# Kernel optimization log

Measured on AMD Instinct MI355X. Metric: run time of the kernel, lower is better.

Reference implementation:

```python
import jax, jax.numpy as jnp
import numpy as np

MG = (5, 5)          # mesh_grid_size
UP = (17, 17)        # upsample_size
IMG = (512.0, 512.0) # image_size
B = 8192
FC_OUT = MG[0] * MG[1] * 2  # 50
KH = (UP[0] - 1) // (MG[0] - 1) + 1  # 5
KW = (UP[1] - 1) // (MG[1] - 1) + 1  # 5
SH = (UP[0] - 1) // (MG[0] - 1)      # 4
SW = (UP[1] - 1) // (MG[1] - 1)      # 4
L0 = MG[0] - 1
L1 = MG[1] - 1


def _grid(h, w):
    # channel 0: x coords vary along rows (image_size[0]); channel 1: y along cols
    x_t = jnp.broadcast_to(jnp.linspace(0.0, IMG[0], h)[:, None], (h, w))
    y_t = jnp.broadcast_to(jnp.linspace(0.0, IMG[1], w)[None, :], (h, w))
    return jnp.stack([x_t, y_t], 0)  # [2, h, w]


def _unfold22(a):
    # a: [B, 2, H, W] -> [B, (H-1)*(W-1), 4, 2]; 4 = kernel positions row-major, 2 = channel
    p = jnp.stack([a[:, :, :-1, :-1], a[:, :, :-1, 1:],
                   a[:, :, 1:, :-1], a[:, :, 1:, 1:]], axis=2)  # [B,2,4,H-1,W-1]
    return p.reshape(a.shape[0], 2, 4, -1).transpose(0, 3, 2, 1)


def _persp(src, dst):
    # exact 4-point homography solve (torchgeometry.get_perspective_transform)
    x0, y0 = src[..., 0], src[..., 1]
    u, v = dst[..., 0], dst[..., 1]
    z = jnp.zeros_like(x0)
    o = jnp.ones_like(x0)
    ax = jnp.stack([x0, y0, o, z, z, z, -u * x0, -u * y0], -1)  # [N,4,8]
    ay = jnp.stack([z, z, z, x0, y0, o, -v * x0, -v * y0], -1)
    A = jnp.concatenate([ax, ay], 1)                 # [N,8,8]
    bb = jnp.concatenate([u, v], 1)[..., None]       # [N,8,1]
    h = jnp.linalg.solve(A, bb)[..., 0]              # [N,8]
    return jnp.concatenate([h, o[:, :1]], 1).reshape(-1, 3, 3)


def setup_inputs() -> dict:
    key = jax.random.key(0)
    ks = jax.random.split(key, 4)
    def lin(k, i, o):
        return jax.random.normal(k, (i, o), jnp.float32) / jnp.sqrt(i)
    return {
        "x": jax.random.normal(ks[0], (B, 1024), jnp.float32),
        "W1": lin(ks[1], 1024, 1024), "b1": jnp.zeros((1024,), jnp.float32),
        "W2": lin(ks[2], 1024, 2048), "b2": jnp.zeros((2048,), jnp.float32),
        "W3": lin(ks[3], 2048, FC_OUT), "b3": jnp.zeros((FC_OUT,), jnp.float32),
    }


def reference(x, W1, b1, W2, b2, W3, b3):
    Bn = x.shape[0]
    h = jax.nn.relu(x @ W1 + b1)
    h = jax.nn.relu(h @ W2 + b2)
    out = (h @ W3 + b3).reshape(Bn, 2, MG[0], MG[1])  # [B,2,5,5] mesh flow

    # sparse control grid and 2x2 patch corner points
    gs = _grid(MG[0], MG[1])
    src = _unfold22(jnp.broadcast_to(gs[None], (Bn, 2, MG[0], MG[1]))).reshape(-1, 4, 2)
    flow = _unfold22(out).reshape(-1, 4, 2)
    M = _persp(src, src + flow)  # [B*16, 3, 3]

    # dense grid and its unfold2 (kernel KHxKW, stride SHxSW) patch points
    gd = _grid(UP[0], UP[1])  # [2, 17, 17]
    gi = (np.arange(L0) * SH)[:, None, None, None] + np.arange(KH)[None, None, :, None]
    gj = (np.arange(L1) * SW)[None, :, None, None] + np.arange(KW)[None, None, None, :]
    I, J = np.broadcast_arrays(gi, gj)  # [L0,L1,KH,KW]
    pts = gd[:, I, J].transpose(1, 2, 3, 4, 0).reshape(1, L0 * L1, KH * KW, 2)
    pts = jnp.broadcast_to(pts, (Bn, L0 * L1, KH * KW, 2)).reshape(Bn * L0 * L1, KH * KW, 2)

    # transform_points: homogeneous warp + perspective divide
    ph = jnp.concatenate([pts, jnp.ones(pts.shape[:-1] + (1,), pts.dtype)], -1)
    oh = jnp.einsum('nij,npj->npi', M, ph)
    warped = oh[..., :2] / oh[..., 2:3]
    warped = warped.reshape(Bn, L0, L1, KH, KW, 2)

    # Fold: scatter-accumulate overlapping patches
    fold = jnp.zeros((Bn, 2, UP[0], UP[1]), x.dtype)
    for i in range(L0):
        for j in range(L1):
            blk = warped[:, i, j].transpose(0, 3, 1, 2)  # [B,2,KH,KW]
            fold = fold.at[:, :, i * SH:i * SH + KH, j * SW:j * SW + KW].add(blk)

    # boundary rescaling exactly as the torch code: only the 5x5 crossing points
    idx = np.arange(0, UP[0], MG[0] - 1)
    X, Y = np.meshgrid(idx, idx, indexing='xy')
    fold = fold.at[:, :, X, Y].multiply(0.5)
    for (a, b) in ((0, 0), (0, UP[1] - 1), (UP[0] - 1, UP[1] - 1), (UP[0] - 1, 0)):
        fold = fold.at[:, :, a, b].multiply(2.0)

    return fold - gd[None]  # upsampled mesh flow [B,2,17,17]
```

## Files before the change

### kernel.cpp

```cpp
#include <hip/hip_runtime.h>

typedef __bf16 bf16x8 __attribute__((ext_vector_type(8)));
typedef float f32x4 __attribute__((ext_vector_type(4)));

__device__ __forceinline__ unsigned short f2bf(float f) {
  unsigned int u = __builtin_bit_cast(unsigned int, f);
  unsigned int r = (u + 0x7fffu + ((u >> 16) & 1u)) >> 16;
  return (unsigned short)r;
}

__device__ __forceinline__ void load16_lds(const unsigned short* g, unsigned short* l) {
  __builtin_amdgcn_global_load_lds(
      (const __attribute__((address_space(1))) void*)g,
      (__attribute__((address_space(3))) void*)l, 16, 0, 0);
}


__global__ __launch_bounds__(256) void prepass(
    const float* __restrict__ x, const float* __restrict__ W1,
    const float* __restrict__ W2, const float* __restrict__ W3,
    unsigned short* __restrict__ xbf, unsigned short* __restrict__ w1t,
    unsigned short* __restrict__ w2t, unsigned short* __restrict__ w3t) {
  __shared__ float tile[32][33];
  const int bid = blockIdx.x;
  const int t = threadIdx.x;
  if (bid < 2048) {
    for (int i = bid * 256 + t; i < 2097152; i += 2048 * 256) {
      float4 f = ((const float4*)x)[i];
      uint2 o;
      o.x = (unsigned)f2bf(f.x) | ((unsigned)f2bf(f.y) << 16);
      o.y = (unsigned)f2bf(f.z) | ((unsigned)f2bf(f.w) << 16);
      ((uint2*)xbf)[i] = o;
    }
  } else if (bid < 3072) {
    int ti = bid - 2048;
    int n0 = (ti & 31) * 32, k0 = (ti >> 5) * 32;
    int tx = t & 31, ty = t >> 5;
    #pragma unroll
    for (int r = 0; r < 32; r += 8)
      tile[ty + r][tx] = W1[(size_t)(k0 + ty + r) * 1024 + n0 + tx];
    __syncthreads();
    #pragma unroll
    for (int r = 0; r < 32; r += 8)
      w1t[(size_t)(n0 + ty + r) * 1024 + k0 + tx] = f2bf(tile[tx][ty + r]);
  } else if (bid < 5120) {
    int ti = bid - 3072;
    int n0 = (ti & 63) * 32, k0 = (ti >> 6) * 32;
    int tx = t & 31, ty = t >> 5;
    #pragma unroll
    for (int r = 0; r < 32; r += 8)
      tile[ty + r][tx] = W2[(size_t)(k0 + ty + r) * 2048 + n0 + tx];
    __syncthreads();
    #pragma unroll
    for (int r = 0; r < 32; r += 8)
      w2t[(size_t)(n0 + ty + r) * 1024 + k0 + tx] = f2bf(tile[tx][ty + r]);
  } else {
    int idx = (bid - 5120) * 256 + t;
    int n = idx >> 11, k = idx & 2047;
    w3t[idx] = f2bf((n < 50) ? W3[(size_t)k * 50 + n] : 0.f);
  }
}


__global__ __launch_bounds__(256) void gemm_bt_relu(
    const unsigned short* __restrict__ A,
    const unsigned short* __restrict__ Bt,
    const float* __restrict__ bias,
    unsigned short* __restrict__ C,
    int N, int K) {
  __shared__ __align__(16) unsigned short As[128 * 64];
  __shared__ __align__(16) unsigned short Bs[128 * 64];
  const int t = threadIdx.x;
  const int m0 = blockIdx.x * 128;
  const int n0 = blockIdx.y * 128;
  const int lane = t & 63, wv = t >> 6;
  const int l16 = lane & 15, quad = lane >> 4;
  const int wm = (wv >> 1) * 64, wn = (wv & 1) * 64;

  const int srow = t >> 3;
  const int scol = ((t & 7) ^ (srow & 7)) * 8;
  const unsigned short* Ag0 = A + (size_t)(m0 + srow) * K + scol;
  const unsigned short* Bg0 = Bt + (size_t)(n0 + srow) * K + scol;
  unsigned short* AsW = As + wv * 8 * 64;
  unsigned short* BsW = Bs + wv * 8 * 64;

  f32x4 acc[4][4] = {};

  for (int k0 = 0; k0 < K; k0 += 64) {
    #pragma unroll
    for (int r = 0; r < 4; ++r) {
      load16_lds(Ag0 + (size_t)(r * 32) * K + k0, AsW + r * 32 * 64);
      load16_lds(Bg0 + (size_t)(r * 32) * K + k0, BsW + r * 32 * 64);
    }
    __syncthreads();
    #pragma unroll
    for (int half = 0; half < 2; ++half) {
      bf16x8 af[4], bfr[4];
      #pragma unroll
      for (int mi = 0; mi < 4; ++mi) {
        int row = wm + mi * 16 + l16;
        int pb = (half * 4 + quad) ^ (row & 7);
        af[mi] = *(const bf16x8*)&As[row * 64 + pb * 8];
      }
      #pragma unroll
      for (int ni = 0; ni < 4; ++ni) {
        int row = wn + ni * 16 + l16;
        int pb = (half * 4 + quad) ^ (row & 7);
        bfr[ni] = *(const bf16x8*)&Bs[row * 64 + pb * 8];
      }
      #pragma unroll
      for (int mi = 0; mi < 4; ++mi)
        #pragma unroll
        for (int ni = 0; ni < 4; ++ni)
          acc[mi][ni] = __builtin_amdgcn_mfma_f32_16x16x32_bf16(
              af[mi], bfr[ni], acc[mi][ni], 0, 0, 0);
    }
    __syncthreads();
  }

  #pragma unroll
  for (int mi = 0; mi < 4; ++mi) {
    #pragma unroll
    for (int ni = 0; ni < 4; ++ni) {
      int col = n0 + wn + ni * 16 + l16;
      float bv = bias[col];
      #pragma unroll
      for (int r = 0; r < 4; ++r) {
        int row = m0 + wm + mi * 16 + quad * 4 + r;
        float v = acc[mi][ni][r] + bv;
        v = fmaxf(v, 0.f);
        C[(size_t)row * N + col] = f2bf(v);
      }
    }
  }
}


__global__ __launch_bounds__(256) void gemm_bt_relu_n64(
    const unsigned short* __restrict__ A,
    const unsigned short* __restrict__ Bt,
    const float* __restrict__ bias,
    unsigned short* __restrict__ C,
    int N, int K) {
  __shared__ __align__(16) unsigned short As[128 * 64];
  __shared__ __align__(16) unsigned short Bs[64 * 64];
  const int t = threadIdx.x;
  const int m0 = blockIdx.x * 128;
  const int n0 = blockIdx.y * 64;
  const int lane = t & 63, wv = t >> 6;
  const int l16 = lane & 15, quad = lane >> 4;
  const int wm = (wv >> 1) * 64, wn = (wv & 1) * 32;

  const int srow = t >> 3;
  const int scol = ((t & 7) ^ (srow & 7)) * 8;
  const unsigned short* Ag0 = A + (size_t)(m0 + srow) * K + scol;
  const unsigned short* Bg0 = Bt + (size_t)(n0 + srow) * K + scol;
  unsigned short* AsW = As + wv * 8 * 64;
  unsigned short* BsW = Bs + wv * 8 * 64;

  f32x4 acc[4][2] = {};

  for (int k0 = 0; k0 < K; k0 += 64) {
    #pragma unroll
    for (int r = 0; r < 4; ++r)
      load16_lds(Ag0 + (size_t)(r * 32) * K + k0, AsW + r * 32 * 64);
    #pragma unroll
    for (int r = 0; r < 2; ++r)
      load16_lds(Bg0 + (size_t)(r * 32) * K + k0, BsW + r * 32 * 64);
    __syncthreads();
    #pragma unroll
    for (int half = 0; half < 2; ++half) {
      bf16x8 af[4], bfr[2];
      #pragma unroll
      for (int mi = 0; mi < 4; ++mi) {
        int row = wm + mi * 16 + l16;
        int pb = (half * 4 + quad) ^ (row & 7);
        af[mi] = *(const bf16x8*)&As[row * 64 + pb * 8];
      }
      #pragma unroll
      for (int ni = 0; ni < 2; ++ni) {
        int row = wn + ni * 16 + l16;
        int pb = (half * 4 + quad) ^ (row & 7);
        bfr[ni] = *(const bf16x8*)&Bs[row * 64 + pb * 8];
      }
      #pragma unroll
      for (int mi = 0; mi < 4; ++mi)
        #pragma unroll
        for (int ni = 0; ni < 2; ++ni)
          acc[mi][ni] = __builtin_amdgcn_mfma_f32_16x16x32_bf16(
              af[mi], bfr[ni], acc[mi][ni], 0, 0, 0);
    }
    __syncthreads();
  }

  #pragma unroll
  for (int mi = 0; mi < 4; ++mi) {
    #pragma unroll
    for (int ni = 0; ni < 2; ++ni) {
      int col = n0 + wn + ni * 16 + l16;
      float bv = bias[col];
      #pragma unroll
      for (int r = 0; r < 4; ++r) {
        int row = m0 + wm + mi * 16 + quad * 4 + r;
        float v = acc[mi][ni][r] + bv;
        v = fmaxf(v, 0.f);
        C[(size_t)row * N + col] = f2bf(v);
      }
    }
  }
}


__global__ __launch_bounds__(256) void gemm3_geom(
    const unsigned short* __restrict__ A,
    const unsigned short* __restrict__ Bt,
    const float* __restrict__ b3,
    float* __restrict__ outp) {
  __shared__ __align__(16) unsigned short As[16 * 64];
  __shared__ __align__(16) unsigned short Bs[64 * 64];
  __shared__ float s_out3[16 * 64];
  __shared__ float s_bias[64];
  __shared__ float fold[16 * 578];
  const int t = threadIdx.x;
  const int lane = t & 63, wv = t >> 6;
  const int l16 = lane & 15, quad = lane >> 4;
  const int m0 = blockIdx.x * 16;

  if (t < 64) s_bias[t] = (t < 50) ? b3[t] : 0.f;
  for (int i = t; i < 16 * 578; i += 256) fold[i] = 0.f;

  const int srow = lane >> 3;
  const int sg = lane & 7;

  f32x4 acc = {};

  for (int k0 = 0; k0 < 2048; k0 += 64) {
    if (wv < 2) {
      int row = wv * 8 + srow;
      int col = (sg ^ (row & 7)) * 8;
      load16_lds(A + (size_t)(m0 + row) * 2048 + k0 + col, As + wv * 8 * 64);
    }
    #pragma unroll
    for (int r = 0; r < 2; ++r) {
      int row = wv * 16 + r * 8 + srow;
      int col = (sg ^ (row & 7)) * 8;
      load16_lds(Bt + (size_t)row * 2048 + k0 + col, Bs + (wv * 16 + r * 8) * 64);
    }
    __syncthreads();
    #pragma unroll
    for (int half = 0; half < 2; ++half) {
      int apb = (half * 4 + quad) ^ (l16 & 7);
      bf16x8 af = *(const bf16x8*)&As[l16 * 64 + apb * 8];
      int brow = wv * 16 + l16;
      int bpb = (half * 4 + quad) ^ (brow & 7);
      bf16x8 bf = *(const bf16x8*)&Bs[brow * 64 + bpb * 8];
      acc = __builtin_amdgcn_mfma_f32_16x16x32_bf16(af, bf, acc, 0, 0, 0);
    }
    __syncthreads();
  }

  {
    int n = wv * 16 + l16;
    float bv = s_bias[n];
    #pragma unroll
    for (int r = 0; r < 4; ++r)
      s_out3[(quad * 4 + r) * 64 + n] = acc[r] + bv;
  }
  __syncthreads();

  {
    const int bl = t >> 4;
    const int p = t & 15;
    const int pi = p >> 2, pj = p & 3;
    const float* o = &s_out3[bl * 64];

    float u00 = 128.f * pi       + o[pi * 5 + pj];
    float v00 = 128.f * pj       + o[25 + pi * 5 + pj];
    float u01 = 128.f * pi       + o[pi * 5 + pj + 1];
    float v01 = 128.f * (pj + 1) + o[25 + pi * 5 + pj + 1];
    float u10 = 128.f * (pi + 1) + o[(pi + 1) * 5 + pj];
    float v10 = 128.f * pj       + o[25 + (pi + 1) * 5 + pj];
    float u11 = 128.f * (pi + 1) + o[(pi + 1) * 5 + pj + 1];
    float v11 = 128.f * (pj + 1) + o[25 + (pi + 1) * 5 + pj + 1];

    float sx = u00 - u10 + u11 - u01;
    float sy = v00 - v10 + v11 - v01;
    float dx1 = u10 - u11, dx2 = u01 - u11;
    float dy1 = v10 - v11, dy2 = v01 - v11;
    float rden = 1.f / (dx1 * dy2 - dx2 * dy1);
    float g = (sx * dy2 - dx2 * sy) * rden;
    float h = (dx1 * sy - sx * dy1) * rden;
    float a = u10 - u00 + g * u10;
    float b = u01 - u00 + h * u01;
    float c = u00;
    float d = v10 - v00 + g * v10;
    float e = v01 - v00 + h * v01;
    float f = v00;

    #pragma unroll
    for (int ai = 0; ai < 5; ++ai) {
      #pragma unroll
      for (int bi = 0; bi < 5; ++bi) {
        float s = 0.25f * ai, tt = 0.25f * bi;
        float rw = 1.f / (g * s + h * tt + 1.f);
        float xx = (a * s + b * tt + c) * rw;
        float yy = (d * s + e * tt + f) * rw;
        int gi = pi * 4 + ai, gj = pj * 4 + bi;
        atomicAdd(&fold[(bl * 2 + 0) * 289 + gi * 17 + gj], xx);
        atomicAdd(&fold[(bl * 2 + 1) * 289 + gi * 17 + gj], yy);
      }
    }
  }
  __syncthreads();

  for (int i = t; i < 16 * 578; i += 256) {
    int blb = i / 578;
    int rem = i - blb * 578;
    int ch = rem / 289;
    int ij = rem - ch * 289;
    int gi = ij / 17, gj = ij - gi * 17;
    float val = fold[i];
    if ((gi % 4 == 0) && (gj % 4 == 0)) val *= 0.5f;
    if ((gi == 0 || gi == 16) && (gj == 0 || gj == 16)) val *= 2.f;
    val -= (ch == 0) ? 32.f * gi : 32.f * gj;
    outp[(size_t)(m0 + blb) * 578 + rem] = val;
  }
}


extern "C" void kernel_launch(void* const* d_in, const int* in_sizes, int n_in,
                              void* d_out, int out_size, void* d_ws, size_t ws_size,
                              hipStream_t stream) {
  const float* x  = (const float*)d_in[0];
  const float* W1 = (const float*)d_in[1];
  const float* b1 = (const float*)d_in[2];
  const float* W2 = (const float*)d_in[3];
  const float* b2 = (const float*)d_in[4];
  const float* W3 = (const float*)d_in[5];
  const float* b3 = (const float*)d_in[6];
  float* outp = (float*)d_out;

  char* ws = (char*)d_ws;
  size_t off = 0;
  auto alloc = [&](size_t bytes) {
    void* pp = ws + off;
    off += (bytes + 255) & ~(size_t)255;
    return pp;
  };
  unsigned short* xbf = (unsigned short*)alloc((size_t)8192 * 1024 * 2);
  unsigned short* w1t = (unsigned short*)alloc((size_t)1024 * 1024 * 2);
  unsigned short* w2t = (unsigned short*)alloc((size_t)2048 * 1024 * 2);
  unsigned short* w3t = (unsigned short*)alloc((size_t)64 * 2048 * 2);
  unsigned short* h1  = (unsigned short*)alloc((size_t)8192 * 1024 * 2);
  unsigned short* h2  = (unsigned short*)alloc((size_t)8192 * 2048 * 2);

  prepass<<<5632, 256, 0, stream>>>(x, W1, W2, W3, xbf, w1t, w2t, w3t);

  gemm_bt_relu_n64<<<dim3(64, 16), 256, 0, stream>>>(xbf, w1t, b1, h1, 1024, 1024);
  gemm_bt_relu<<<dim3(64, 16), 256, 0, stream>>>(h1, w2t, b2, h2, 2048, 1024);
  gemm3_geom<<<512, 256, 0, stream>>>(h2, w3t, b3, outp);
}
```

Before: 219.3 us.

## Split third GEMM into split-K tiled kernel plus separate geometry reduce kernel

```diff
diff --git a/kernel.cpp b/kernel.cpp
--- a/kernel.cpp
+++ b/kernel.cpp
@@ -211,60 +211,92 @@
 }
 
 
-__global__ __launch_bounds__(256) void gemm3_geom(
+__global__ __launch_bounds__(256) void gemm3_part(
     const unsigned short* __restrict__ A,
     const unsigned short* __restrict__ Bt,
-    const float* __restrict__ b3,
-    float* __restrict__ outp) {
-  __shared__ __align__(16) unsigned short As[16 * 64];
+    float* __restrict__ part) {
+  __shared__ __align__(16) unsigned short As[128 * 64];
   __shared__ __align__(16) unsigned short Bs[64 * 64];
-  __shared__ float s_out3[16 * 64];
-  __shared__ float s_bias[64];
-  __shared__ float fold[16 * 578];
-  const int t = threadIdx.x;
+  const int t = threadIdx.x;
+  const int m0 = blockIdx.x * 128;
+  const int kz = blockIdx.y;
   const int lane = t & 63, wv = t >> 6;
   const int l16 = lane & 15, quad = lane >> 4;
-  const int m0 = blockIdx.x * 16;
-
-  if (t < 64) s_bias[t] = (t < 50) ? b3[t] : 0.f;
+  const int wm = (wv >> 1) * 64, wn = (wv & 1) * 32;
+
+  const int srow = t >> 3;
+  const int scol = ((t & 7) ^ (srow & 7)) * 8;
+  const unsigned short* Ag0 = A + (size_t)(m0 + srow) * 2048 + kz * 512 + scol;
+  const unsigned short* Bg0 = Bt + (size_t)srow * 2048 + kz * 512 + scol;
+  unsigned short* AsW = As + wv * 8 * 64;
+  unsigned short* BsW = Bs + wv * 8 * 64;
+
+  f32x4 acc[4][2] = {};
+
+  for (int k0 = 0; k0 < 512; k0 += 64) {
+    #pragma unroll
+    for (int r = 0; r < 4; ++r)
+      load16_lds(Ag0 + (size_t)(r * 32) * 2048 + k0, AsW + r * 32 * 64);
+    #pragma unroll
+    for (int r = 0; r < 2; ++r)
+      load16_lds(Bg0 + (size_t)(r * 32) * 2048 + k0, BsW + r * 32 * 64);
+    __syncthreads();
+    #pragma unroll
+    for (int half = 0; half < 2; ++half) {
+      bf16x8 af[4], bfr[2];
+      #pragma unroll
+      for (int mi = 0; mi < 4; ++mi) {
+        int row = wm + mi * 16 + l16;
+        int pb = (half * 4 + quad) ^ (row & 7);
+        af[mi] = *(const bf16x8*)&As[row * 64 + pb * 8];
+      }
+      #pragma unroll
+      for (int ni = 0; ni < 2; ++ni) {
+        int row = wn + ni * 16 + l16;
+        int pb = (half * 4 + quad) ^ (row & 7);
+        bfr[ni] = *(const bf16x8*)&Bs[row * 64 + pb * 8];
+      }
+      #pragma unroll
+      for (int mi = 0; mi < 4; ++mi)
+        #pragma unroll
+        for (int ni = 0; ni < 2; ++ni)
+          acc[mi][ni] = __builtin_amdgcn_mfma_f32_16x16x32_bf16(
+              af[mi], bfr[ni], acc[mi][ni], 0, 0, 0);
+    }
+    __syncthreads();
+  }
+
+  float* pbase = part + (size_t)kz * 8192 * 64;
+  #pragma unroll
+  for (int mi = 0; mi < 4; ++mi) {
+    #pragma unroll
+    for (int ni = 0; ni < 2; ++ni) {
+      int col = wn + ni * 16 + l16;
+      #pragma unroll
+      for (int r = 0; r < 4; ++r) {
+        int row = m0 + wm + mi * 16 + quad * 4 + r;
+        pbase[(size_t)row * 64 + col] = acc[mi][ni][r];
+      }
+    }
+  }
+}
+
+
+__global__ __launch_bounds__(256) void geom_reduce(
+    const float* __restrict__ part, const float* __restrict__ b3,
+    float* __restrict__ outp) {
+  __shared__ float s_out3[16 * 64];
+  __shared__ float fold[16 * 578];
+  const int t = threadIdx.x;
+  const int bbase = blockIdx.x * 16;
+
   for (int i = t; i < 16 * 578; i += 256) fold[i] = 0.f;
-
-  const int srow = lane >> 3;
-  const int sg = lane & 7;
-
-  f32x4 acc = {};
-
-  for (int k0 = 0; k0 < 2048; k0 += 64) {
-    if (wv < 2) {
-      int row = wv * 8 + srow;
-      int col = (sg ^ (row & 7)) * 8;
-      load16_lds(A + (size_t)(m0 + row) * 2048 + k0 + col, As + wv * 8 * 64);
-    }
-    #pragma unroll
-    for (int r = 0; r < 2; ++r) {
-      int row = wv * 16 + r * 8 + srow;
-      int col = (sg ^ (row & 7)) * 8;
-      load16_lds(Bt + (size_t)row * 2048 + k0 + col, Bs + (wv * 16 + r * 8) * 64);
-    }
-    __syncthreads();
-    #pragma unroll
-    for (int half = 0; half < 2; ++half) {
-      int apb = (half * 4 + quad) ^ (l16 & 7);
-      bf16x8 af = *(const bf16x8*)&As[l16 * 64 + apb * 8];
-      int brow = wv * 16 + l16;
-      int bpb = (half * 4 + quad) ^ (brow & 7);
-      bf16x8 bf = *(const bf16x8*)&Bs[brow * 64 + bpb * 8];
-      acc = __builtin_amdgcn_mfma_f32_16x16x32_bf16(af, bf, acc, 0, 0, 0);
-    }
-    __syncthreads();
-  }
-
-  {
-    int n = wv * 16 + l16;
-    float bv = s_bias[n];
-    #pragma unroll
-    for (int r = 0; r < 4; ++r)
-      s_out3[(quad * 4 + r) * 64 + n] = acc[r] + bv;
+  for (int i = t; i < 1024; i += 256) {
+    int m = i >> 6, n = i & 63;
+    size_t idx = (size_t)(bbase + m) * 64 + n;
+    float v = part[idx] + part[idx + (size_t)8192 * 64]
+            + part[idx + (size_t)2 * 8192 * 64] + part[idx + (size_t)3 * 8192 * 64];
+    s_out3[i] = v + ((n < 50) ? b3[n] : 0.f);
   }
   __syncthreads();
 
@@ -323,7 +355,7 @@
     if ((gi % 4 == 0) && (gj % 4 == 0)) val *= 0.5f;
     if ((gi == 0 || gi == 16) && (gj == 0 || gj == 16)) val *= 2.f;
     val -= (ch == 0) ? 32.f * gi : 32.f * gj;
-    outp[(size_t)(m0 + blb) * 578 + rem] = val;
+    outp[(size_t)(bbase + blb) * 578 + rem] = val;
   }
 }
 
@@ -353,10 +385,12 @@
   unsigned short* w3t = (unsigned short*)alloc((size_t)64 * 2048 * 2);
   unsigned short* h1  = (unsigned short*)alloc((size_t)8192 * 1024 * 2);
   unsigned short* h2  = (unsigned short*)alloc((size_t)8192 * 2048 * 2);
+  float* part = (float*)alloc((size_t)4 * 8192 * 64 * 4);
 
   prepass<<<5632, 256, 0, stream>>>(x, W1, W2, W3, xbf, w1t, w2t, w3t);
 
   gemm_bt_relu_n64<<<dim3(64, 16), 256, 0, stream>>>(xbf, w1t, b1, h1, 1024, 1024);
   gemm_bt_relu<<<dim3(64, 16), 256, 0, stream>>>(h1, w2t, b2, h2, 2048, 1024);
-  gemm3_geom<<<512, 256, 0, stream>>>(h2, w3t, b3, outp);
-}
+  gemm3_part<<<dim3(64, 4), 256, 0, stream>>>(h2, w3t, part);
+  geom_reduce<<<512, 256, 0, stream>>>(part, b3, outp);
+}
```

Result: no change. 219.2 us (-0.0%).

## Double-buffer A tile in LDS, load B to registers, split-K the final GEMM

Applied to the files above, without the earlier changes.

```diff
diff --git a/kernel.cpp b/kernel.cpp
--- a/kernel.cpp
+++ b/kernel.cpp
@@ -62,14 +62,14 @@
 }
 
 
-__global__ __launch_bounds__(256) void gemm_bt_relu(
+__global__ __launch_bounds__(256, 4) void gemm_pipe(
     const unsigned short* __restrict__ A,
     const unsigned short* __restrict__ Bt,
     const float* __restrict__ bias,
     unsigned short* __restrict__ C,
-    int N, int K) {
-  __shared__ __align__(16) unsigned short As[128 * 64];
-  __shared__ __align__(16) unsigned short Bs[128 * 64];
+    int N) {
+  constexpr int K = 1024;
+  __shared__ __align__(16) unsigned short As[2 * 128 * 64];
   const int t = threadIdx.x;
   const int m0 = blockIdx.x * 128;
   const int n0 = blockIdx.y * 128;
@@ -79,100 +79,111 @@
 
   const int srow = t >> 3;
   const int scol = ((t & 7) ^ (srow & 7)) * 8;
-  const unsigned short* Ag0 = A + (size_t)(m0 + srow) * K + scol;
-  const unsigned short* Bg0 = Bt + (size_t)(n0 + srow) * K + scol;
-  unsigned short* AsW = As + wv * 8 * 64;
-  unsigned short* BsW = Bs + wv * 8 * 64;
+  const unsigned short* Ag = A + (size_t)(m0 + srow) * K + scol;
+  unsigned short* AsW = As + wv * 512;
+
+  const unsigned short* Bg = Bt + (size_t)(n0 + wn + l16) * K + quad * 8;
 
   f32x4 acc[4][4] = {};
 
-  for (int k0 = 0; k0 < K; k0 += 64) {
-    #pragma unroll
-    for (int r = 0; r < 4; ++r) {
-      load16_lds(Ag0 + (size_t)(r * 32) * K + k0, AsW + r * 32 * 64);
-      load16_lds(Bg0 + (size_t)(r * 32) * K + k0, BsW + r * 32 * 64);
-    }
-    __syncthreads();
+  #pragma unroll
+  for (int r = 0; r < 4; ++r)
+    load16_lds(Ag + (size_t)(r * 32) * K, AsW + r * 2048);
+  __syncthreads();
+
+  for (int i = 0; i < 16; ++i) {
+    const int k = i * 64;
+    const int cur = (i & 1) * 8192, nxt = 8192 - cur;
+    if (i < 15) {
+      #pragma unroll
+      for (int r = 0; r < 4; ++r)
+        load16_lds(Ag + (size_t)(r * 32) * K + k + 64, AsW + nxt + r * 2048);
+    }
+    bf16x8 bqa[4], bqb[4];
+    #pragma unroll
+    for (int ni = 0; ni < 4; ++ni) {
+      const unsigned short* bp = Bg + (size_t)(ni * 16) * K + k;
+      bqa[ni] = *(const bf16x8*)bp;
+      bqb[ni] = *(const bf16x8*)(bp + 32);
+    }
     #pragma unroll
     for (int half = 0; half < 2; ++half) {
-      bf16x8 af[4], bfr[4];
+      bf16x8 af[4];
       #pragma unroll
       for (int mi = 0; mi < 4; ++mi) {
         int row = wm + mi * 16 + l16;
         int pb = (half * 4 + quad) ^ (row & 7);
-        af[mi] = *(const bf16x8*)&As[row * 64 + pb * 8];
-      }
-      #pragma unroll
-      for (int ni = 0; ni < 4; ++ni) {
-        int row = wn + ni * 16 + l16;
-        int pb = (half * 4 + quad) ^ (row & 7);
-        bfr[ni] = *(const bf16x8*)&Bs[row * 64 + pb * 8];
+        af[mi] = *(const bf16x8*)&As[cur + row * 64 + pb * 8];
       }
       #pragma unroll
       for (int mi = 0; mi < 4; ++mi)
         #pragma unroll
         for (int ni = 0; ni < 4; ++ni)
           acc[mi][ni] = __builtin_amdgcn_mfma_f32_16x16x32_bf16(
-              af[mi], bfr[ni], acc[mi][ni], 0, 0, 0);
-    }
-    __syncthreads();
-  }
-
+              af[mi], half ? bqb[ni] : bqa[ni], acc[mi][ni], 0, 0, 0);
+    }
+    __syncthreads();
+  }
+
+  unsigned short* Cs = As;
   #pragma unroll
-  for (int mi = 0; mi < 4; ++mi) {
-    #pragma unroll
-    for (int ni = 0; ni < 4; ++ni) {
-      int col = n0 + wn + ni * 16 + l16;
-      float bv = bias[col];
+  for (int ni = 0; ni < 4; ++ni) {
+    int col = wn + ni * 16 + l16;
+    float bv = bias[n0 + col];
+    #pragma unroll
+    for (int mi = 0; mi < 4; ++mi) {
       #pragma unroll
       for (int r = 0; r < 4; ++r) {
-        int row = m0 + wm + mi * 16 + quad * 4 + r;
-        float v = acc[mi][ni][r] + bv;
-        v = fmaxf(v, 0.f);
-        C[(size_t)row * N + col] = f2bf(v);
-      }
-    }
-  }
-}
-
-
-__global__ __launch_bounds__(256) void gemm_bt_relu_n64(
+        int row = wm + mi * 16 + quad * 4 + r;
+        Cs[row * 128 + col] = f2bf(fmaxf(acc[mi][ni][r] + bv, 0.f));
+      }
+    }
+  }
+  __syncthreads();
+  #pragma unroll
+  for (int j = 0; j < 8; ++j) {
+    int idx = j * 256 + t;
+    int row = idx >> 4;
+    int cc = (idx & 15) * 8;
+    *(uint4*)&C[(size_t)(m0 + row) * N + n0 + cc] = *(const uint4*)&Cs[row * 128 + cc];
+  }
+}
+
+
+__global__ __launch_bounds__(256) void gemm3_part(
     const unsigned short* __restrict__ A,
     const unsigned short* __restrict__ Bt,
-    const float* __restrict__ bias,
-    unsigned short* __restrict__ C,
-    int N, int K) {
-  __shared__ __align__(16) unsigned short As[128 * 64];
+    float* __restrict__ part) {
+  __shared__ __align__(16) unsigned short As[64 * 64];
   __shared__ __align__(16) unsigned short Bs[64 * 64];
   const int t = threadIdx.x;
-  const int m0 = blockIdx.x * 128;
-  const int n0 = blockIdx.y * 64;
+  const int m0 = blockIdx.x * 64;
+  const int kz = blockIdx.y;
   const int lane = t & 63, wv = t >> 6;
   const int l16 = lane & 15, quad = lane >> 4;
-  const int wm = (wv >> 1) * 64, wn = (wv & 1) * 32;
+  const int wm = (wv >> 1) * 32, wn = (wv & 1) * 32;
 
   const int srow = t >> 3;
   const int scol = ((t & 7) ^ (srow & 7)) * 8;
-  const unsigned short* Ag0 = A + (size_t)(m0 + srow) * K + scol;
-  const unsigned short* Bg0 = Bt + (size_t)(n0 + srow) * K + scol;
-  unsigned short* AsW = As + wv * 8 * 64;
-  unsigned short* BsW = Bs + wv * 8 * 64;
-
-  f32x4 acc[4][2] = {};
-
-  for (int k0 = 0; k0 < K; k0 += 64) {
-    #pragma unroll
-    for (int r = 0; r < 4; ++r)
-      load16_lds(Ag0 + (size_t)(r * 32) * K + k0, AsW + r * 32 * 64);
-    #pragma unroll
-    for (int r = 0; r < 2; ++r)
-      load16_lds(Bg0 + (size_t)(r * 32) * K + k0, BsW + r * 32 * 64);
+  const unsigned short* Ag = A + (size_t)(m0 + srow) * 2048 + kz * 256 + scol;
+  const unsigned short* Bg = Bt + (size_t)srow * 2048 + kz * 256 + scol;
+  unsigned short* AsW = As + wv * 512;
+  unsigned short* BsW = Bs + wv * 512;
+
+  f32x4 acc[2][2] = {};
+
+  for (int k0 = 0; k0 < 256; k0 += 64) {
+    #pragma unroll
+    for (int r = 0; r < 2; ++r) {
+      load16_lds(Ag + (size_t)(r * 32) * 2048 + k0, AsW + r * 2048);
+      load16_lds(Bg + (size_t)(r * 32) * 2048 + k0, BsW + r * 2048);
+    }
     __syncthreads();
     #pragma unroll
     for (int half = 0; half < 2; ++half) {
-      bf16x8 af[4], bfr[2];
-      #pragma unroll
-      for (int mi = 0; mi < 4; ++mi) {
+      bf16x8 af[2], bfr[2];
+      #pragma unroll
+      for (int mi = 0; mi < 2; ++mi) {
         int row = wm + mi * 16 + l16;
         int pb = (half * 4 + quad) ^ (row & 7);
         af[mi] = *(const bf16x8*)&As[row * 64 + pb * 8];
@@ -184,7 +195,7 @@
         bfr[ni] = *(const bf16x8*)&Bs[row * 64 + pb * 8];
       }
       #pragma unroll
-      for (int mi = 0; mi < 4; ++mi)
+      for (int mi = 0; mi < 2; ++mi)
         #pragma unroll
         for (int ni = 0; ni < 2; ++ni)
           acc[mi][ni] = __builtin_amdgcn_mfma_f32_16x16x32_bf16(
@@ -193,78 +204,38 @@
     __syncthreads();
   }
 
+  float* pbase = part + (size_t)kz * 8192 * 64;
   #pragma unroll
-  for (int mi = 0; mi < 4; ++mi) {
+  for (int mi = 0; mi < 2; ++mi) {
     #pragma unroll
     for (int ni = 0; ni < 2; ++ni) {
-      int col = n0 + wn + ni * 16 + l16;
-      float bv = bias[col];
+      int col = wn + ni * 16 + l16;
       #pragma unroll
       for (int r = 0; r < 4; ++r) {
         int row = m0 + wm + mi * 16 + quad * 4 + r;
-        float v = acc[mi][ni][r] + bv;
-        v = fmaxf(v, 0.f);
-        C[(size_t)row * N + col] = f2bf(v);
-      }
-    }
-  }
-}
-
-
-__global__ __launch_bounds__(256) void gemm3_geom(
-    const unsigned short* __restrict__ A,
-    const unsigned short* __restrict__ Bt,
-    const float* __restrict__ b3,
+        pbase[(size_t)row * 64 + col] = acc[mi][ni][r];
+      }
+    }
+  }
+}
+
+
+__global__ __launch_bounds__(256) void geom_reduce(
+    const float* __restrict__ part, const float* __restrict__ b3,
     float* __restrict__ outp) {
-  __shared__ __align__(16) unsigned short As[16 * 64];
-  __shared__ __align__(16) unsigned short Bs[64 * 64];
   __shared__ float s_out3[16 * 64];
-  __shared__ float s_bias[64];
   __shared__ float fold[16 * 578];
   const int t = threadIdx.x;
-  const int lane = t & 63, wv = t >> 6;
-  const int l16 = lane & 15, quad = lane >> 4;
-  const int m0 = blockIdx.x * 16;
-
-  if (t < 64) s_bias[t] = (t < 50) ? b3[t] : 0.f;
+  const int bbase = blockIdx.x * 16;
+
   for (int i = t; i < 16 * 578; i += 256) fold[i] = 0.f;
-
-  const int srow = lane >> 3;
-  const int sg = lane & 7;
-
-  f32x4 acc = {};
-
-  for (int k0 = 0; k0 < 2048; k0 += 64) {
-    if (wv < 2) {
-      int row = wv * 8 + srow;
-      int col = (sg ^ (row & 7)) * 8;
-      load16_lds(A + (size_t)(m0 + row) * 2048 + k0 + col, As + wv * 8 * 64);
-    }
-    #pragma unroll
-    for (int r = 0; r < 2; ++r) {
-      int row = wv * 16 + r * 8 + srow;
-      int col = (sg ^ (row & 7)) * 8;
-      load16_lds(Bt + (size_t)row * 2048 + k0 + col, Bs + (wv * 16 + r * 8) * 64);
-    }
-    __syncthreads();
-    #pragma unroll
-    for (int half = 0; half < 2; ++half) {
-      int apb = (half * 4 + quad) ^ (l16 & 7);
-      bf16x8 af = *(const bf16x8*)&As[l16 * 64 + apb * 8];
-      int brow = wv * 16 + l16;
-      int bpb = (half * 4 + quad) ^ (brow & 7);
-      bf16x8 bf = *(const bf16x8*)&Bs[brow * 64 + bpb * 8];
-      acc = __builtin_amdgcn_mfma_f32_16x16x32_bf16(af, bf, acc, 0, 0, 0);
-    }
-    __syncthreads();
-  }
-
-  {
-    int n = wv * 16 + l16;
-    float bv = s_bias[n];
-    #pragma unroll
-    for (int r = 0; r < 4; ++r)
-      s_out3[(quad * 4 + r) * 64 + n] = acc[r] + bv;
+  for (int i = t; i < 1024; i += 256) {
+    int m = i >> 6, n = i & 63;
+    size_t idx = (size_t)(bbase + m) * 64 + n;
+    float v = 0.f;
+    #pragma unroll
+    for (int z = 0; z < 8; ++z) v += part[idx + (size_t)z * 8192 * 64];
+    s_out3[i] = v + ((n < 50) ? b3[n] : 0.f);
   }
   __syncthreads();
 
@@ -323,7 +294,7 @@
     if ((gi % 4 == 0) && (gj % 4 == 0)) val *= 0.5f;
     if ((gi == 0 || gi == 16) && (gj == 0 || gj == 16)) val *= 2.f;
     val -= (ch == 0) ? 32.f * gi : 32.f * gj;
-    outp[(size_t)(m0 + blb) * 578 + rem] = val;
+    outp[(size_t)(bbase + blb) * 578 + rem] = val;
   }
 }
 
@@ -341,22 +312,19 @@
   float* outp = (float*)d_out;
 
   char* ws = (char*)d_ws;
-  size_t off = 0;
-  auto alloc = [&](size_t bytes) {
-    void* pp = ws + off;
-    off += (bytes + 255) & ~(size_t)255;
-    return pp;
-  };
-  unsigned short* xbf = (unsigned short*)alloc((size_t)8192 * 1024 * 2);
-  unsigned short* w1t = (unsigned short*)alloc((size_t)1024 * 1024 * 2);
-  unsigned short* w2t = (unsigned short*)alloc((size_t)2048 * 1024 * 2);
-  unsigned short* w3t = (unsigned short*)alloc((size_t)64 * 2048 * 2);
-  unsigned short* h1  = (unsigned short*)alloc((size_t)8192 * 1024 * 2);
-  unsigned short* h2  = (unsigned short*)alloc((size_t)8192 * 2048 * 2);
+  unsigned short* h2  = (unsigned short*)ws;
+  unsigned short* xbf = (unsigned short*)ws;
+  unsigned short* w1t = (unsigned short*)(ws + (size_t)16 * 1024 * 1024);
+  unsigned short* w2t = (unsigned short*)(ws + (size_t)32 * 1024 * 1024);
+  unsigned short* w3t = (unsigned short*)(ws + (size_t)36 * 1024 * 1024);
+  char* tail = ws + (size_t)36 * 1024 * 1024 + 512 * 1024;
+  unsigned short* h1  = (unsigned short*)tail;
+  float* part = (float*)tail;
 
   prepass<<<5632, 256, 0, stream>>>(x, W1, W2, W3, xbf, w1t, w2t, w3t);
 
-  gemm_bt_relu_n64<<<dim3(64, 16), 256, 0, stream>>>(xbf, w1t, b1, h1, 1024, 1024);
-  gemm_bt_relu<<<dim3(64, 16), 256, 0, stream>>>(h1, w2t, b2, h2, 2048, 1024);
-  gemm3_geom<<<512, 256, 0, stream>>>(h2, w3t, b3, outp);
-}
+  gemm_pipe<<<dim3(64, 8), 256, 0, stream>>>(xbf, w1t, b1, h1, 1024);
+  gemm_pipe<<<dim3(64, 16), 256, 0, stream>>>(h1, w2t, b2, h2, 2048);
+  gemm3_part<<<dim3(128, 8), 256, 0, stream>>>(h2, w3t, part);
+  geom_reduce<<<512, 256, 0, stream>>>(part, b3, outp);
+}
```

Measured after the change: 257.6 us. 17.5% more time.
